# Performance work log

Hardware: AMD Instinct MI355X
Metric: run time of the kernel (lower is better)

Reference implementation:

```python
import jax, jax.numpy as jnp
import numpy as np

N_NODES = 100000
N_EDGES = 3200000
IN_DIM, HID, OUT_DIM = 512, 64, 5


def _glorot(key, shape):
    fan_in, fan_out = shape[0], shape[1]
    lim = np.sqrt(6.0 / (fan_in + fan_out))
    return jax.random.uniform(key, shape, jnp.float32, -lim, lim)


def setup_inputs() -> dict:
    key = jax.random.key(0)
    ks = jax.random.split(key, 10)
    x = jax.random.normal(ks[0], (N_NODES, IN_DIM), jnp.float32)
    edge_index = jax.random.randint(ks[1], (2, N_EDGES), 0, N_NODES, jnp.int64)
    edge_weight = jax.random.uniform(ks[2], (N_EDGES,), jnp.float32)
    return {
        "x": x,
        "edge_index": edge_index,
        "edge_weight": edge_weight,
        "W1": _glorot(ks[3], (IN_DIM, HID)),
        "b1": jnp.zeros((HID,), jnp.float32),
        "W2": _glorot(ks[4], (HID, HID)),
        "b2": jnp.zeros((HID,), jnp.float32),
        "Wfc": _glorot(ks[5], (HID, OUT_DIM)),
        "bfc": jnp.zeros((OUT_DIM,), jnp.float32),
    }


def _gcn_norm(edge_index, edge_weight, num_nodes):
    # PyG gcn_norm: add self-loops (weight 1), symmetric deg^-1/2 normalization.
    loop = jnp.arange(num_nodes, dtype=edge_index.dtype)
    src = jnp.concatenate([edge_index[0], loop])
    dst = jnp.concatenate([edge_index[1], loop])
    ew = jnp.concatenate([edge_weight, jnp.ones((num_nodes,), edge_weight.dtype)])
    deg = jax.ops.segment_sum(ew, dst, num_segments=num_nodes)
    dinv = jnp.where(deg > 0, jax.lax.rsqrt(deg), 0.0)
    norm = dinv[src] * ew * dinv[dst]
    return src, dst, norm


def _gcn_conv(x, W, b, src, dst, norm, num_nodes):
    h = x @ W  # transform first (GCNConv does lin before propagate)
    msg = norm[:, None] * h[src]  # gather + scale  [E, d]
    out = jax.ops.segment_sum(msg, dst, num_segments=num_nodes)  # scatter-add
    return out + b


def reference(x, edge_index, edge_weight, W1, b1, W2, b2, Wfc, bfc):
    n = x.shape[0]
    src, dst, norm = _gcn_norm(edge_index, edge_weight, n)
    h = jax.nn.relu(_gcn_conv(x, W1, b1, src, dst, norm, n))
    h = jax.nn.relu(_gcn_conv(h, W2, b2, src, dst, norm, n))
    return h @ Wfc + bfc
```

## Files before the change

kernel.cpp:

```cpp
#include <hip/hip_runtime.h>

#define IN_DIM 512
#define HID 64
#define OUT_DIM 5


__device__ __forceinline__ unsigned short f2bf(float f) {
    unsigned u = __float_as_uint(f);
    u += 0x7FFF + ((u >> 16) & 1);
    return (unsigned short)(u >> 16);
}
__device__ __forceinline__ float bf2f(unsigned short b) {
    return __uint_as_float(((unsigned)b) << 16);
}


__global__ void k_init(unsigned long long* __restrict__ packed, int n) {
    int i = blockIdx.x * blockDim.x + threadIdx.x;
    if (i < n) packed[i] = 0ULL;
}


__launch_bounds__(256)
__global__ void k_gemm1_hist(const float* __restrict__ A, const float* __restrict__ W,
                             float* __restrict__ out, unsigned short* __restrict__ outb, int M,
                             const int* __restrict__ dst, const float* __restrict__ ew,
                             unsigned long long* __restrict__ packed, int* __restrict__ rank,
                             int nE, int gemmBlocks) {
    if ((int)blockIdx.x < gemmBlocks) {
        constexpr int K_ = IN_DIM;
        constexpr int BK = 16;
        __shared__ float As[BK][68];
        __shared__ float Ws[BK][64];

        const int t  = threadIdx.x;
        const int tx = t & 15;
        const int ty = t >> 4;
        const int row0 = blockIdx.x * 64;

        const int lr = t >> 2;
        const int lk = (t & 3) * 4;

        float acc[4][4] = {};

        for (int k0 = 0; k0 < K_; k0 += BK) {
            float4 av = make_float4(0.f, 0.f, 0.f, 0.f);
            int ar = row0 + lr;
            if (ar < M) av = *(const float4*)&A[(long long)ar * K_ + k0 + lk];
            As[lk + 0][lr] = av.x;
            As[lk + 1][lr] = av.y;
            As[lk + 2][lr] = av.z;
            As[lk + 3][lr] = av.w;

            *(float4*)&Ws[t >> 4][(t & 15) * 4] =
                *(const float4*)&W[(long long)(k0 + (t >> 4)) * 64 + (t & 15) * 4];

            __syncthreads();

#pragma unroll
            for (int kk = 0; kk < BK; ++kk) {
                float4 a4 = *(const float4*)&As[kk][ty * 4];
                float4 b4 = *(const float4*)&Ws[kk][tx * 4];
                float a[4] = {a4.x, a4.y, a4.z, a4.w};
                float b[4] = {b4.x, b4.y, b4.z, b4.w};
#pragma unroll
                for (int i = 0; i < 4; ++i)
#pragma unroll
                    for (int j = 0; j < 4; ++j)
                        acc[i][j] = fmaf(a[i], b[j], acc[i][j]);
            }
            __syncthreads();
        }

#pragma unroll
        for (int i = 0; i < 4; ++i) {
            int r = row0 + ty * 4 + i;
            if (r < M) {
                *(float4*)&out[(long long)r * 64 + tx * 4] =
                    make_float4(acc[i][0], acc[i][1], acc[i][2], acc[i][3]);
                ushort4 hv;
                hv.x = f2bf(acc[i][0]);
                hv.y = f2bf(acc[i][1]);
                hv.z = f2bf(acc[i][2]);
                hv.w = f2bf(acc[i][3]);
                *(ushort4*)&outb[(long long)r * 64 + tx * 4] = hv;
            }
        }
    } else {
        int base = ((blockIdx.x - gemmBlocks) * 256 + threadIdx.x) * 4;
        if (base + 3 < nE) {
            int4   d4 = *(const int4*)&dst[base];
            float4 w4 = *(const float4*)&ew[base];
            unsigned long long f0 = (unsigned long long)(w4.x * 4294967296.0);
            unsigned long long f1 = (unsigned long long)(w4.y * 4294967296.0);
            unsigned long long f2 = (unsigned long long)(w4.z * 4294967296.0);
            unsigned long long f3 = (unsigned long long)(w4.w * 4294967296.0);
            unsigned long long o0 = atomicAdd(&packed[d4.x], (1ULL << 44) | f0);
            unsigned long long o1 = atomicAdd(&packed[d4.y], (1ULL << 44) | f1);
            unsigned long long o2 = atomicAdd(&packed[d4.z], (1ULL << 44) | f2);
            unsigned long long o3 = atomicAdd(&packed[d4.w], (1ULL << 44) | f3);
            int4 r4;
            r4.x = (int)(o0 >> 44);
            r4.y = (int)(o1 >> 44);
            r4.z = (int)(o2 >> 44);
            r4.w = (int)(o3 >> 44);
            *(int4*)&rank[base] = r4;
        } else {
            for (int e = base; e < nE; ++e) {
                int d = dst[e];
                unsigned long long fx = (unsigned long long)(ew[e] * 4294967296.0);
                unsigned long long old = atomicAdd(&packed[d], (1ULL << 44) | fx);
                rank[e] = (int)(old >> 44);
            }
        }
    }
}


__global__ void k_scan1d(const unsigned long long* __restrict__ packed,
                         float* __restrict__ dinv, int* __restrict__ rowptr,
                         int* __restrict__ bsum, int n) {
    __shared__ int sdata[256];
    int t = threadIdx.x, b = blockIdx.x;
    int base = b * 1024 + t * 4;
    int v[4], s = 0;
#pragma unroll
    for (int k = 0; k < 4; ++k) {
        int i = base + k;
        int c = 0;
        if (i < n) {
            unsigned long long p = packed[i];
            c = (int)(p >> 44);
            double ewsum = (double)(p & ((1ULL << 44) - 1)) * (1.0 / 4294967296.0);
            dinv[i] = rsqrtf(1.0f + (float)ewsum);
        }
        v[k] = c;
        s += c;
    }
    sdata[t] = s;
    __syncthreads();
    int x = s;
    for (int off = 1; off < 256; off <<= 1) {
        int y = (t >= off) ? sdata[t - off] : 0;
        __syncthreads();
        x += y;
        sdata[t] = x;
        __syncthreads();
    }
    int run = x - s;
    if (t == 255) bsum[b] = x;
#pragma unroll
    for (int k = 0; k < 4; ++k) { int i = base + k; if (i < n) rowptr[i] = run; run += v[k]; }
}

__global__ void k_scan2(int* __restrict__ bsum, int nb) {
    __shared__ int sdata[256];
    int t = threadIdx.x;
    int s = (t < nb) ? bsum[t] : 0;
    sdata[t] = s;
    __syncthreads();
    int x = s;
    for (int off = 1; off < 256; off <<= 1) {
        int y = (t >= off) ? sdata[t - off] : 0;
        __syncthreads();
        x += y;
        sdata[t] = x;
        __syncthreads();
    }
    if (t < nb) bsum[t] = x - s;
}

__global__ void k_scan3(int* __restrict__ rowptr, const int* __restrict__ bsum, int n, int E) {
    int i = blockIdx.x * blockDim.x + threadIdx.x;
    if (i < n) rowptr[i] += bsum[i >> 10];
    else if (i == n) rowptr[n] = E;
}


__global__ void k_reorder(const int* __restrict__ src, const int* __restrict__ dst,
                          const float* __restrict__ ew, const float* __restrict__ dinv,
                          const int* __restrict__ rowptr, const int* __restrict__ rank,
                          int2* __restrict__ edges, int nE) {
    int e = blockIdx.x * blockDim.x + threadIdx.x;
    if (e < nE) {
        int s = src[e];
        int d = dst[e];
        float w = dinv[s] * ew[e] * dinv[d];
        int pos = rowptr[d] + rank[e];
        edges[pos] = make_int2(s, __float_as_int(w));
    }
}


__launch_bounds__(256)
__global__ void k_aggregate(const float* __restrict__ h, const unsigned short* __restrict__ hb,
                            const float* __restrict__ dinv,
                            const int2* __restrict__ edges, const int* __restrict__ rowptr,
                            float* __restrict__ out, int N) {
    int n = (blockIdx.x * 256 + threadIdx.x) >> 6;
    int lane = threadIdx.x & 63;
    if (n >= N) return;

    float dn = dinv[n];
    float acc = dn * dn * h[(size_t)n * HID + lane];

    int beg = rowptr[n], end = rowptr[n + 1];
    int j = beg;
    for (; j + 7 < end; j += 8) {
        int2 p0 = edges[j];
        int2 p1 = edges[j + 1];
        int2 p2 = edges[j + 2];
        int2 p3 = edges[j + 3];
        int2 p4 = edges[j + 4];
        int2 p5 = edges[j + 5];
        int2 p6 = edges[j + 6];
        int2 p7 = edges[j + 7];
        float h0 = bf2f(hb[(size_t)p0.x * HID + lane]);
        float h1 = bf2f(hb[(size_t)p1.x * HID + lane]);
        float h2 = bf2f(hb[(size_t)p2.x * HID + lane]);
        float h3 = bf2f(hb[(size_t)p3.x * HID + lane]);
        float h4 = bf2f(hb[(size_t)p4.x * HID + lane]);
        float h5 = bf2f(hb[(size_t)p5.x * HID + lane]);
        float h6 = bf2f(hb[(size_t)p6.x * HID + lane]);
        float h7 = bf2f(hb[(size_t)p7.x * HID + lane]);
        acc = fmaf(__int_as_float(p0.y), h0, acc);
        acc = fmaf(__int_as_float(p1.y), h1, acc);
        acc = fmaf(__int_as_float(p2.y), h2, acc);
        acc = fmaf(__int_as_float(p3.y), h3, acc);
        acc = fmaf(__int_as_float(p4.y), h4, acc);
        acc = fmaf(__int_as_float(p5.y), h5, acc);
        acc = fmaf(__int_as_float(p6.y), h6, acc);
        acc = fmaf(__int_as_float(p7.y), h7, acc);
    }
    for (; j < end; ++j) {
        int2 p = edges[j];
        acc = fmaf(__int_as_float(p.y), bf2f(hb[(size_t)p.x * HID + lane]), acc);
    }
    out[(size_t)n * HID + lane] = acc;
}


template <int K_, bool RELU_BIAS>
__launch_bounds__(256)
__global__ void k_gemm_n64(const float* __restrict__ A, const float* __restrict__ W,
                           const float* __restrict__ bias, float* __restrict__ out,
                           unsigned short* __restrict__ outb, int M) {
    constexpr int BK = 16;
    __shared__ float As[BK][68];
    __shared__ float Ws[BK][64];

    const int t  = threadIdx.x;
    const int tx = t & 15;
    const int ty = t >> 4;
    const int row0 = blockIdx.x * 64;

    const int lr = t >> 2;
    const int lk = (t & 3) * 4;

    float acc[4][4] = {};

    for (int k0 = 0; k0 < K_; k0 += BK) {
        float4 av = make_float4(0.f, 0.f, 0.f, 0.f);
        int ar = row0 + lr;
        if (ar < M) {
            av = *(const float4*)&A[(long long)ar * K_ + k0 + lk];
            if (RELU_BIAS) {
                const float4 bv = *(const float4*)&bias[k0 + lk];
                av.x = fmaxf(av.x + bv.x, 0.f);
                av.y = fmaxf(av.y + bv.y, 0.f);
                av.z = fmaxf(av.z + bv.z, 0.f);
                av.w = fmaxf(av.w + bv.w, 0.f);
            }
        }
        As[lk + 0][lr] = av.x;
        As[lk + 1][lr] = av.y;
        As[lk + 2][lr] = av.z;
        As[lk + 3][lr] = av.w;

        *(float4*)&Ws[t >> 4][(t & 15) * 4] =
            *(const float4*)&W[(long long)(k0 + (t >> 4)) * 64 + (t & 15) * 4];

        __syncthreads();

#pragma unroll
        for (int kk = 0; kk < BK; ++kk) {
            float4 a4 = *(const float4*)&As[kk][ty * 4];
            float4 b4 = *(const float4*)&Ws[kk][tx * 4];
            float a[4] = {a4.x, a4.y, a4.z, a4.w};
            float b[4] = {b4.x, b4.y, b4.z, b4.w};
#pragma unroll
            for (int i = 0; i < 4; ++i)
#pragma unroll
                for (int j = 0; j < 4; ++j)
                    acc[i][j] = fmaf(a[i], b[j], acc[i][j]);
        }
        __syncthreads();
    }

#pragma unroll
    for (int i = 0; i < 4; ++i) {
        int r = row0 + ty * 4 + i;
        if (r < M) {
            *(float4*)&out[(long long)r * 64 + tx * 4] =
                make_float4(acc[i][0], acc[i][1], acc[i][2], acc[i][3]);
            ushort4 hv;
            hv.x = f2bf(acc[i][0]);
            hv.y = f2bf(acc[i][1]);
            hv.z = f2bf(acc[i][2]);
            hv.w = f2bf(acc[i][3]);
            *(ushort4*)&outb[(long long)r * 64 + tx * 4] = hv;
        }
    }
}


__launch_bounds__(256)
__global__ void k_final(const float* __restrict__ agg, const float* __restrict__ b2,
                        const float* __restrict__ Wfc, const float* __restrict__ bfc,
                        float* __restrict__ out, int N) {
    __shared__ float Wsf[HID * OUT_DIM];
    __shared__ float bs[HID];
    int t = threadIdx.x;
    for (int i = t; i < HID * OUT_DIM; i += 256) Wsf[i] = Wfc[i];
    if (t < HID) bs[t] = b2[t];
    __syncthreads();

    int n = blockIdx.x * blockDim.x + t;
    if (n >= N) return;

    float acc[OUT_DIM];
#pragma unroll
    for (int o = 0; o < OUT_DIM; ++o) acc[o] = bfc[o];

    const float4* ag = (const float4*)&agg[(long long)n * HID];
#pragma unroll
    for (int k4 = 0; k4 < HID / 4; ++k4) {
        float4 v4 = ag[k4];
        float v[4] = {v4.x, v4.y, v4.z, v4.w};
#pragma unroll
        for (int j = 0; j < 4; ++j) {
            int k = k4 * 4 + j;
            float f = fmaxf(v[j] + bs[k], 0.f);
#pragma unroll
            for (int o = 0; o < OUT_DIM; ++o)
                acc[o] = fmaf(f, Wsf[k * OUT_DIM + o], acc[o]);
        }
    }
#pragma unroll
    for (int o = 0; o < OUT_DIM; ++o) out[(long long)n * OUT_DIM + o] = acc[o];
}


static inline size_t align_up(size_t x, size_t a) { return (x + a - 1) & ~(a - 1); }

extern "C" void kernel_launch(void* const* d_in, const int* in_sizes, int n_in,
                              void* d_out, int out_size, void* d_ws, size_t ws_size,
                              hipStream_t stream) {
    const float* x   = (const float*)d_in[0];
    const int*   ei  = (const int*)d_in[1];
    const float* ew  = (const float*)d_in[2];
    const float* W1  = (const float*)d_in[3];
    const float* b1  = (const float*)d_in[4];
    const float* W2  = (const float*)d_in[5];
    const float* b2  = (const float*)d_in[6];
    const float* Wfc = (const float*)d_in[7];
    const float* bfc = (const float*)d_in[8];
    float* out = (float*)d_out;

    const int E = in_sizes[2];
    const int N = in_sizes[0] / IN_DIM;
    const int* src = ei;
    const int* dst = ei + E;

    char* p = (char*)d_ws;
    unsigned long long* packed = (unsigned long long*)p; p += align_up((size_t)N * 8, 256);
    float* dinv   = (float*)p;  p += align_up((size_t)N * 4, 256);
    int*   rowptr = (int*)p;    p += align_up((size_t)(N + 1) * 4, 256);
    int*   bsum   = (int*)p;    p += align_up((size_t)256 * 4, 256);
    unsigned short* hb = (unsigned short*)p; p += align_up((size_t)N * HID * 2, 256);
    int2*  edges  = (int2*)p;   p += align_up((size_t)E * 8, 256);
    float* bufA   = (float*)p;  p += align_up((size_t)N * HID * 4, 256);
    float* bufB   = (float*)p;  p += align_up((size_t)N * HID * 4, 256);
    int*   rank   = (int*)bufB;
    (void)ws_size; (void)n_in; (void)out_size;

    const int BS = 256;
    dim3 blk(BS);
    int gN  = (N + BS - 1) / BS;
    int gN1 = (N + 1 + BS - 1) / BS;
    int gE  = (E + BS - 1) / BS;
    int gE4 = (E + BS * 4 - 1) / (BS * 4);
    int gM  = (N + 63) / 64;
    int nb  = (N + 1023) / 1024;
    int gAg = (N + 3) / 4;

    k_init<<<gN, blk, 0, stream>>>(packed, N);
    k_gemm1_hist<<<gM + gE4, blk, 0, stream>>>(x, W1, bufA, hb, N,
                                               dst, ew, packed, rank, E, gM);
    k_scan1d<<<nb, blk, 0, stream>>>(packed, dinv, rowptr, bsum, N);
    k_scan2<<<1, blk, 0, stream>>>(bsum, nb);
    k_scan3<<<gN1, blk, 0, stream>>>(rowptr, bsum, N, E);
    k_reorder<<<gE, blk, 0, stream>>>(src, dst, ew, dinv, rowptr, rank, edges, E);

    k_aggregate<<<gAg, blk, 0, stream>>>(bufA, hb, dinv, edges, rowptr, bufB, N);

    k_gemm_n64<HID, true><<<gM, blk, 0, stream>>>(bufB, W2, b1, bufA, hb, N);
    k_aggregate<<<gAg, blk, 0, stream>>>(bufA, hb, dinv, edges, rowptr, bufB, N);

    k_final<<<gN, blk, 0, stream>>>(bufB, b2, Wfc, bfc, out, N);
}
```

Baseline: 748.0 us.

## Privatize degree histogram into eight copies to reduce atomic contention

The packed count/weight histogram is replicated eight times, and each histogram block atomically adds into the copy chosen by its block index. The scan kernel then sums the copies, computes per-copy prefix offsets and stores them as 16-bit values per node, which the reorder kernel adds when placing each edge. The aim is to spread same-address 64-bit atomics across copies and cut contention. In exchange it zero-fills, reads and writes eight times the histogram memory and adds an extra offset lookup per edge in the reorder step.

```diff
diff --git a/kernel.cpp b/kernel.cpp
--- a/kernel.cpp
+++ b/kernel.cpp
@@ -3,6 +3,7 @@
 #define IN_DIM 512
 #define HID 64
 #define OUT_DIM 5
+#define NCOPY 8
 
 
 __device__ __forceinline__ unsigned short f2bf(float f) {
@@ -15,9 +16,9 @@
 }
 
 
-__global__ void k_init(unsigned long long* __restrict__ packed, int n) {
+__global__ void k_init(unsigned long long* __restrict__ packed, int n8) {
     int i = blockIdx.x * blockDim.x + threadIdx.x;
-    if (i < n) packed[i] = 0ULL;
+    if (i < n8) packed[i] = 0ULL;
 }
 
 
@@ -87,7 +88,9 @@
             }
         }
     } else {
-        int base = ((blockIdx.x - gemmBlocks) * 256 + threadIdx.x) * 4;
+        const int hb = (int)blockIdx.x - gemmBlocks;
+        unsigned long long* __restrict__ pk = packed + (size_t)(hb & (NCOPY - 1)) * M;
+        int base = hb * 1024 + threadIdx.x * 4;
         if (base + 3 < nE) {
             int4   d4 = *(const int4*)&dst[base];
             float4 w4 = *(const float4*)&ew[base];
@@ -95,10 +98,10 @@
             unsigned long long f1 = (unsigned long long)(w4.y * 4294967296.0);
             unsigned long long f2 = (unsigned long long)(w4.z * 4294967296.0);
             unsigned long long f3 = (unsigned long long)(w4.w * 4294967296.0);
-            unsigned long long o0 = atomicAdd(&packed[d4.x], (1ULL << 44) | f0);
-            unsigned long long o1 = atomicAdd(&packed[d4.y], (1ULL << 44) | f1);
-            unsigned long long o2 = atomicAdd(&packed[d4.z], (1ULL << 44) | f2);
-            unsigned long long o3 = atomicAdd(&packed[d4.w], (1ULL << 44) | f3);
+            unsigned long long o0 = atomicAdd(&pk[d4.x], (1ULL << 44) | f0);
+            unsigned long long o1 = atomicAdd(&pk[d4.y], (1ULL << 44) | f1);
+            unsigned long long o2 = atomicAdd(&pk[d4.z], (1ULL << 44) | f2);
+            unsigned long long o3 = atomicAdd(&pk[d4.w], (1ULL << 44) | f3);
             int4 r4;
             r4.x = (int)(o0 >> 44);
             r4.y = (int)(o1 >> 44);
@@ -109,7 +112,7 @@
             for (int e = base; e < nE; ++e) {
                 int d = dst[e];
                 unsigned long long fx = (unsigned long long)(ew[e] * 4294967296.0);
-                unsigned long long old = atomicAdd(&packed[d], (1ULL << 44) | fx);
+                unsigned long long old = atomicAdd(&pk[d], (1ULL << 44) | fx);
                 rank[e] = (int)(old >> 44);
             }
         }
@@ -119,7 +122,7 @@
 
 __global__ void k_scan1d(const unsigned long long* __restrict__ packed,
                          float* __restrict__ dinv, int* __restrict__ rowptr,
-                         int* __restrict__ bsum, int n) {
+                         int* __restrict__ bsum, unsigned short* __restrict__ coff, int n) {
     __shared__ int sdata[256];
     int t = threadIdx.x, b = blockIdx.x;
     int base = b * 1024 + t * 4;
@@ -127,15 +130,28 @@
 #pragma unroll
     for (int k = 0; k < 4; ++k) {
         int i = base + k;
-        int c = 0;
+        int cnt = 0;
         if (i < n) {
-            unsigned long long p = packed[i];
-            c = (int)(p >> 44);
-            double ewsum = (double)(p & ((1ULL << 44) - 1)) * (1.0 / 4294967296.0);
-            dinv[i] = rsqrtf(1.0f + (float)ewsum);
-        }
-        v[k] = c;
-        s += c;
+            unsigned long long ewsum = 0;
+            unsigned short cv[NCOPY];
+#pragma unroll
+            for (int c = 0; c < NCOPY; ++c) {
+                unsigned long long pp = packed[(size_t)c * n + i];
+                cv[c] = (unsigned short)cnt;
+                cnt += (int)(pp >> 44);
+                ewsum += pp & ((1ULL << 44) - 1);
+            }
+            double es = (double)ewsum * (1.0 / 4294967296.0);
+            dinv[i] = rsqrtf(1.0f + (float)es);
+            uint4 w;
+            w.x = (unsigned)cv[0] | ((unsigned)cv[1] << 16);
+            w.y = (unsigned)cv[2] | ((unsigned)cv[3] << 16);
+            w.z = (unsigned)cv[4] | ((unsigned)cv[5] << 16);
+            w.w = (unsigned)cv[6] | ((unsigned)cv[7] << 16);
+            *(uint4*)&coff[(size_t)i * NCOPY] = w;
+        }
+        v[k] = cnt;
+        s += cnt;
     }
     sdata[t] = s;
     __syncthreads();
@@ -180,13 +196,15 @@
 __global__ void k_reorder(const int* __restrict__ src, const int* __restrict__ dst,
                           const float* __restrict__ ew, const float* __restrict__ dinv,
                           const int* __restrict__ rowptr, const int* __restrict__ rank,
+                          const unsigned short* __restrict__ coff,
                           int2* __restrict__ edges, int nE) {
     int e = blockIdx.x * blockDim.x + threadIdx.x;
     if (e < nE) {
         int s = src[e];
         int d = dst[e];
+        int c = (e >> 10) & (NCOPY - 1);
         float w = dinv[s] * ew[e] * dinv[d];
-        int pos = rowptr[d] + rank[e];
+        int pos = rowptr[d] + (int)coff[(size_t)d * NCOPY + c] + rank[e];
         edges[pos] = make_int2(s, __float_as_int(w));
     }
 }
@@ -373,7 +391,7 @@
     const int* dst = ei + E;
 
     char* p = (char*)d_ws;
-    unsigned long long* packed = (unsigned long long*)p; p += align_up((size_t)N * 8, 256);
+    unsigned long long* packed = (unsigned long long*)p; p += align_up((size_t)NCOPY * N * 8, 256);
     float* dinv   = (float*)p;  p += align_up((size_t)N * 4, 256);
     int*   rowptr = (int*)p;    p += align_up((size_t)(N + 1) * 4, 256);
     int*   bsum   = (int*)p;    p += align_up((size_t)256 * 4, 256);
@@ -382,11 +400,13 @@
     float* bufA   = (float*)p;  p += align_up((size_t)N * HID * 4, 256);
     float* bufB   = (float*)p;  p += align_up((size_t)N * HID * 4, 256);
     int*   rank   = (int*)bufB;
+    unsigned short* coff = (unsigned short*)((char*)bufB + align_up((size_t)E * 4, 256));
     (void)ws_size; (void)n_in; (void)out_size;
 
     const int BS = 256;
     dim3 blk(BS);
     int gN  = (N + BS - 1) / BS;
+    int gN8 = (NCOPY * N + BS - 1) / BS;
     int gN1 = (N + 1 + BS - 1) / BS;
     int gE  = (E + BS - 1) / BS;
     int gE4 = (E + BS * 4 - 1) / (BS * 4);
@@ -394,13 +414,13 @@
     int nb  = (N + 1023) / 1024;
     int gAg = (N + 3) / 4;
 
-    k_init<<<gN, blk, 0, stream>>>(packed, N);
+    k_init<<<gN8, blk, 0, stream>>>(packed, NCOPY * N);
     k_gemm1_hist<<<gM + gE4, blk, 0, stream>>>(x, W1, bufA, hb, N,
                                                dst, ew, packed, rank, E, gM);
-    k_scan1d<<<nb, blk, 0, stream>>>(packed, dinv, rowptr, bsum, N);
+    k_scan1d<<<nb, blk, 0, stream>>>(packed, dinv, rowptr, bsum, coff, N);
     k_scan2<<<1, blk, 0, stream>>>(bsum, nb);
     k_scan3<<<gN1, blk, 0, stream>>>(rowptr, bsum, N, E);
-    k_reorder<<<gE, blk, 0, stream>>>(src, dst, ew, dinv, rowptr, rank, edges, E);
+    k_reorder<<<gE, blk, 0, stream>>>(src, dst, ew, dinv, rowptr, rank, coff, edges, E);
 
     k_aggregate<<<gAg, blk, 0, stream>>>(bufA, hb, dinv, edges, rowptr, bufB, N);
 
```

Result: slower. 775.9 us (+3.7%).
